# Performance work log

Measured on AMD Instinct MI355X. Metric: run time of the kernel, lower is better.

The kernel has to match this reference:

```python
import jax, jax.numpy as jnp
import numpy as np

R, N, C, E, H, NC = 25, 256, 64, 128, 8, 27


def _layernorm(x, w, b, axes, eps):
    m = x.mean(axis=axes, keepdims=True)
    v = x.var(axis=axes, keepdims=True)
    return (x - m) / jnp.sqrt(v + eps) * w + b


def _mha(emb_ln, idx, WQ, WK):
    # emb_ln: (R*N, E); idx: (L,) district indices
    ew = emb_ln.reshape(R, N, E)[idx]                       # (L,N,E) gather of district blocks
    Q = jnp.einsum('lne,hfe->lhnf', ew, WQ)                 # torch Linear: x @ W.T
    K = jnp.einsum('lne,hfe->lhnf', ew, WK)
    QK = jnp.einsum('lhnf,lhmf->lhnm', Q, K) / jnp.sqrt(jnp.float32(E))
    return jax.nn.softmax(QK, axis=2)                       # torch softmax(dim=1) over (L,n,n)


def setup_inputs() -> dict:
    key = jax.random.key(0)
    ks = jax.random.split(key, 16)
    inp = {
        'business_structure_target': jax.random.normal(ks[0], (R, C, N, 4), jnp.float32),
        'business_structure_infected': jax.random.normal(ks[1], (R, C, N, 4), jnp.float32),
        'customer_structure_target': jax.random.normal(ks[2], (R, C, N, NC, 4), jnp.float32),
        'customer_structure_infected': jax.random.normal(ks[3], (R, C, N, NC, 4), jnp.float32),
        'index_target_idx': jax.random.randint(ks[4], (R, C), 0, R),
        'index_infected_idx': jax.random.randint(ks[5], (R, C), 0, R),
        'covid_outbreak_business': jax.random.randint(ks[6], (R, C), 0, N),
        'emb_table': jax.random.normal(ks[7], (R * N, E), jnp.float32),
        'ln_emb_w': jnp.ones((E,), jnp.float32),
        'ln_emb_b': jnp.zeros((E,), jnp.float32),
        'WQ_trg': jax.random.normal(ks[8], (H, E, E), jnp.float32) * 0.05,
        'WK_trg': jax.random.normal(ks[9], (H, E, E), jnp.float32) * 0.05,
        'WQ_inf': jax.random.normal(ks[10], (H, E, E), jnp.float32) * 0.05,
        'WK_inf': jax.random.normal(ks[11], (H, E, E), jnp.float32) * 0.05,
        'W_os': jax.random.normal(ks[12], (E, E), jnp.float32) * 0.05,
        'b_os': jnp.zeros((E,), jnp.float32),
        'bs_w': jnp.ones((C, N), jnp.float32), 'bs_b': jnp.zeros((C, N), jnp.float32),
        'cs_w': jnp.ones((C, N), jnp.float32), 'cs_b': jnp.zeros((C, N), jnp.float32),
        'os_w': jnp.ones((C, N), jnp.float32), 'os_b': jnp.zeros((C, N), jnp.float32),
    }
    return inp


def reference(business_structure_target, business_structure_infected,
              customer_structure_target, customer_structure_infected,
              index_target_idx, index_infected_idx, covid_outbreak_business,
              emb_table, ln_emb_w, ln_emb_b,
              WQ_trg, WK_trg, WQ_inf, WK_inf,
              W_os, b_os, bs_w, bs_b, cs_w, cs_b, os_w, os_b):
    # mean over feature dim, then slicing per original forward
    bst = business_structure_target.mean(-1)[:R, 0]        # (R,N)
    bsi = business_structure_infected.mean(-1)[0]          # (C,N)
    cst = customer_structure_target.mean(-1)[:R, 0]        # (R,N,NC)
    csi = customer_structure_infected.mean(-1)[0]          # (C,N,NC)

    emb_ln = _layernorm(emb_table, ln_emb_w, ln_emb_b, -1, 1e-16)
    idx_t = index_target_idx[:R, 0]                        # (R,)
    idx_i = index_infected_idx[0]                          # (C,)

    attn_t = _mha(emb_ln, idx_t, WQ_trg, WK_trg)           # (R,H,N,N)
    BR_t = jnp.einsum('ln,lhnm->lmh', bst, attn_t)         # (R,N,H)
    attn_i = _mha(emb_ln, idx_i, WQ_inf, WK_inf)           # (C,H,N,N)
    BR_i = jnp.einsum('cn,chnm->cmh', bsi, attn_i)         # (C,N,H)

    # cosine similarity over head dim, broadcast (R,1,N,H) x (1,C,N,H)
    a = BR_t[:, None]
    b = BR_i[None]
    dot = jnp.sum(a * b, -1)
    na = jnp.linalg.norm(a, axis=-1)
    nb = jnp.linalg.norm(b, axis=-1)
    BS = dot / jnp.maximum(na * nb, 1e-15)                 # (R,C,N)

    # Jensen-Shannon-style KLD over consumer dim (log_target=True semantics)
    log_p = jax.nn.log_softmax(cst, -1)[:, None]           # (R,1,N,NC)
    log_q = jax.nn.log_softmax(csi, -1)[None]              # (1,C,N,NC)
    log_m = jax.nn.log_softmax((log_p + log_q) / 2, -1)
    kl_p = (jnp.exp(log_m) * (log_m - log_p)).mean(-1)
    kl_q = (jnp.exp(log_m) * (log_m - log_q)).mean(-1)
    CS = -(kl_p + kl_q) / 2                                # (R,C,N)

    biz = covid_outbreak_business[0]                       # (C,)
    inf_emb = emb_table[idx_i * N + biz]                   # (C,E) raw (non-LN) embedding
    proj = inf_emb @ W_os.T + b_os
    OS = (proj @ emb_table.T).reshape(C, R, N).transpose(1, 0, 2)  # (R,C,N)

    BS = _layernorm(BS, bs_w, bs_b, (-2, -1), 1e-5)
    CS = _layernorm(CS, cs_w, cs_b, (-2, -1), 1e-5)
    OS = _layernorm(OS, os_w, os_b, (-2, -1), 1e-5)
    return BS, CS, OS
```

## Files before the change

### kernel.cpp

```cpp
#include <hip/hip_runtime.h>
#include <math.h>

#define R_ 25
#define N_ 256
#define C_ 64
#define E_ 128
#define H_ 8
#define NC_ 27
#define SQS 28

typedef _Float16 f16x8 __attribute__((ext_vector_type(8)));
typedef float f32x16 __attribute__((ext_vector_type(16)));

union HU { ushort s; _Float16 h; };
__device__ __forceinline__ ushort ftoh(float f) { HU u; u.h = (_Float16)f; return u.s; }
__device__ __forceinline__ float htof(ushort s) { HU u; u.s = s; return (float)u.h; }

__device__ __forceinline__ float waveReduceSum(float v) {
  #pragma unroll
  for (int off = 32; off > 0; off >>= 1) v += __shfl_xor(v, off);
  return v;
}

__global__ __launch_bounds__(256) void k_prep(
    const float* __restrict__ emb, const float* __restrict__ ln_w,
    const float* __restrict__ ln_b, ushort* __restrict__ emb16,
    const float* __restrict__ bus_t, const float* __restrict__ bus_i,
    float* __restrict__ bst, float* __restrict__ bsi,
    const float* __restrict__ cus_t, const float* __restrict__ cus_i,
    float* __restrict__ Ssq, float* __restrict__ Tsq,
    const int* __restrict__ idx_t, const int* __restrict__ idx_i,
    int* __restrict__ cnt, int* __restrict__ lst,
    const int* __restrict__ biz, const float* __restrict__ Wos,
    const float* __restrict__ bos, float* __restrict__ projb) {
  __shared__ float er2[2][E_];
  int bid = blockIdx.x, t = threadIdx.x;
  if (bid < 1600) {
    int row = bid * 4 + (t >> 6);
    int lane = t & 63;
    const float2* x = (const float2*)(emb + (size_t)row * E_);
    float2 v = x[lane];
    float s = waveReduceSum(v.x + v.y);
    float m = s * (1.0f / 128.0f);
    float d0 = v.x - m, d1 = v.y - m;
    float ss = waveReduceSum(d0 * d0 + d1 * d1);
    float inv = 1.0f / sqrtf(ss * (1.0f / 128.0f) + 1e-16f);
    float2 wv = ((const float2*)ln_w)[lane];
    float2 bv = ((const float2*)ln_b)[lane];
    uint u = (uint)ftoh(d0 * inv * wv.x + bv.x) | ((uint)ftoh(d1 * inv * wv.y + bv.y) << 16);
    ((uint*)emb16)[(size_t)row * 64 + lane] = u;
  } else if (bid < 1689) {
    int i = (bid - 1600) * 256 + t;
    if (i < R_ * N_) {
      size_t row = (size_t)(i >> 8) * (C_ * N_) + (i & 255);
      float4 v = *(const float4*)&bus_t[row * 4];
      bst[i] = (v.x + v.y + v.z + v.w) * 0.25f;
    }
    int j = i - R_ * N_;
    if (j >= 0 && j < C_ * N_) {
      float4 v = *(const float4*)&bus_i[(size_t)j * 4];
      bsi[j] = (v.x + v.y + v.z + v.w) * 0.25f;
    }
  } else if (bid < 1778) {
    int i = (bid - 1689) * 256 + t;
    const float* src; float* dst; size_t base; int oi;
    if (i < R_ * N_) {
      src = cus_t; dst = Ssq; oi = i;
      base = ((size_t)(i >> 8) * (C_ * N_) + (i & 255)) * (NC_ * 4);
    } else {
      int j = i - R_ * N_;
      if (j >= C_ * N_) return;
      src = cus_i; dst = Tsq; oi = j;
      base = ((size_t)(j >> 8) * N_ + (j & 255)) * (NC_ * 4);
    }
    float v[NC_];
    float mx = -1e30f;
    #pragma unroll
    for (int j = 0; j < NC_; ++j) {
      float4 q = *(const float4*)&src[base + j * 4];
      v[j] = (q.x + q.y + q.z + q.w) * 0.25f;
      mx = fmaxf(mx, v[j]);
    }
    float se = 0.0f;
    #pragma unroll
    for (int j = 0; j < NC_; ++j) se += expf(v[j] - mx);
    float lse = mx + logf(se);
    #pragma unroll
    for (int j = 0; j < NC_; ++j) dst[(size_t)oi * SQS + j] = expf(0.5f * (v[j] - lse));
    dst[(size_t)oi * SQS + NC_] = 0.0f;
  } else if (bid == 1778) {
    if (t < 2 * R_) cnt[t] = 0;
    __syncthreads();
    if (t < R_) {
      int rr = idx_t[t * C_];
      int pos = atomicAdd(&cnt[rr], 1);
      lst[rr * 64 + pos] = t;
    }
    if (t < C_) {
      int rr = idx_i[t];
      int pos = atomicAdd(&cnt[R_ + rr], 1);
      lst[(R_ + rr) * 64 + pos] = t;
    }
  } else {
    int pb = bid - 1779;
    int ci = t >> 7, f = t & 127;
    int c = pb * 2 + ci;
    int row = idx_i[c] * N_ + biz[c];
    er2[ci][f] = emb[(size_t)row * E_ + f];
    __syncthreads();
    float acc = bos[f];
    const float* wr = &Wos[(size_t)f * E_];
    const float* er = er2[ci];
    for (int e = 0; e < E_; e += 4) {
      float4 w4 = *(const float4*)&wr[e];
      acc += er[e] * w4.x + er[e + 1] * w4.y + er[e + 2] * w4.z + er[e + 3] * w4.w;
    }
    projb[c * E_ + f] = acc;
  }
}

__global__ __launch_bounds__(512) void k_gt_mfma(
    const float* __restrict__ WQt_, const float* __restrict__ WKt_,
    const float* __restrict__ WQi_, const float* __restrict__ WKi_,
    ushort* __restrict__ Gt) {
  int h = blockIdx.x, set = blockIdx.y;
  const float* WQ = (set ? WQi_ : WQt_) + ((size_t)h << 14);
  const float* WK = (set ? WKi_ : WKt_) + ((size_t)h << 14);
  __shared__ uint QT[128 * 64];
  __shared__ uint KT[128 * 64];
  int t = threadIdx.x;
  for (int j = t; j < 8192; j += 512) {
    int e = j & 127, f2 = j >> 7;
    int wi = (f2 << 8) + e;
    float q0 = WQ[wi], q1 = WQ[wi + 128];
    float k0 = WK[wi], k1 = WK[wi + 128];
    int idx = (e << 6) + (f2 ^ ((e & 15) << 2));
    QT[idx] = (uint)ftoh(q0) | ((uint)ftoh(q1) << 16);
    KT[idx] = (uint)ftoh(k0) | ((uint)ftoh(k1) << 16);
  }
  __syncthreads();
  int w = t >> 6, l = t & 63, lo = l & 31, hi = l >> 5;
  int m0 = (w & 3) << 5, n0 = (w >> 2) << 6;
  f32x16 acc[2];
  #pragma unroll
  for (int i = 0; i < 2; ++i)
    #pragma unroll
    for (int j = 0; j < 16; ++j) acc[i][j] = 0.0f;
  int mrow = m0 + lo;
  #pragma unroll
  for (int ks = 0; ks < 8; ++ks) {
    int f2b = (ks << 3) + (hi << 2);
    f16x8 a = *(const f16x8*)&KT[(mrow << 6) + (f2b ^ ((mrow & 15) << 2))];
    #pragma unroll
    for (int tl = 0; tl < 2; ++tl) {
      int ncol = n0 + (tl << 5) + lo;
      f16x8 b = *(const f16x8*)&QT[(ncol << 6) + (f2b ^ ((ncol & 15) << 2))];
      acc[tl] = __builtin_amdgcn_mfma_f32_32x32x16_f16(a, b, acc[tl], 0, 0, 0);
    }
  }
  const float scale = 0.08838834764831845f;
  ushort* Go = Gt + (((size_t)(set * H_ + h)) << 14);
  #pragma unroll
  for (int tl = 0; tl < 2; ++tl)
    #pragma unroll
    for (int rg = 0; rg < 16; ++rg) {
      int row = m0 + (rg & 3) + ((rg >> 2) << 3) + (hi << 2);
      int col = n0 + (tl << 5) + lo;
      Go[(row << 7) + col] = ftoh(acc[tl][rg] * scale);
    }
}

__global__ __launch_bounds__(512) void k_attn_fused(
    const ushort* __restrict__ emb16, const ushort* __restrict__ GtAll,
    const int* __restrict__ cnt, const int* __restrict__ lst,
    const float* __restrict__ bst, const float* __restrict__ bsi,
    float* __restrict__ BRt, float* __restrict__ BRi) {
  int r = blockIdx.x, h = blockIdx.y, set = blockIdx.z;
  int g = set * R_ + r;
  int L = cnt[g];
  if (L == 0) return;
  __shared__ ushort ELN[256 * 128];
  __shared__ ushort TA[128 * 128];
  __shared__ ushort TB[128 * 128];
  __shared__ float redA[8 * 128];
  __shared__ float redB[8 * 128];
  __shared__ float gM[128], gD[128];
  int t = threadIdx.x;
  const uint4* Ep = (const uint4*)(emb16 + ((size_t)r << 15));
  for (int c = t; c < 4096; c += 512) {
    int n = c >> 4, s = c & 15;
    uint4 v = Ep[c];
    *(uint4*)&ELN[(n << 7) + ((s << 3) ^ ((n & 15) << 3))] = v;
  }
  const uint4* Gp = (const uint4*)(GtAll + ((size_t)(set * H_ + h) << 14));
  for (int c = t; c < 2048; c += 512) {
    int e2 = c >> 4, s = c & 15;
    uint4 v = Gp[c];
    *(uint4*)&TA[(e2 << 7) + ((s << 3) ^ ((e2 & 15) << 3))] = v;
  }
  __syncthreads();
  int w = t >> 6, l = t & 63, lo = l & 31, hi = l >> 5;
  f32x16 tacc[4];
  #pragma unroll
  for (int i = 0; i < 4; ++i)
    #pragma unroll
    for (int j = 0; j < 16; ++j) tacc[i][j] = 0.0f;
  int n = (w << 5) + lo;
  #pragma unroll
  for (int ks = 0; ks < 8; ++ks) {
    f16x8 a = *(const f16x8*)&ELN[(n << 7) + (((ks << 4) + (hi << 3)) ^ ((n & 15) << 3))];
    #pragma unroll
    for (int tl = 0; tl < 4; ++tl) {
      int f = (tl << 5) + lo;
      f16x8 b = *(const f16x8*)&TA[(f << 7) + (((ks << 4) + (hi << 3)) ^ ((f & 15) << 3))];
      tacc[tl] = __builtin_amdgcn_mfma_f32_32x32x16_f16(a, b, tacc[tl], 0, 0, 0);
    }
  }
  __syncthreads();
  {
    ushort* Tl = (w < 4) ? TA : TB;
    #pragma unroll
    for (int tl = 0; tl < 4; ++tl)
      #pragma unroll
      for (int rg = 0; rg < 16; ++rg) {
        int row = ((w & 3) << 5) + (rg & 3) + ((rg >> 2) << 3) + (hi << 2);
        int col = (tl << 5) + lo;
        Tl[(row << 7) + (col ^ ((row & 15) << 3))] = ftoh(tacc[tl][rg]);
      }
  }
  __syncthreads();
  const float* wv = set ? bsi : bst;
  float* BR = set ? BRi : BRt;
  const ushort* Tl = (w < 4) ? TA : TB;
  int rrow = n & 127;
  int baseRow = (w << 5) + (hi << 2);
  for (int mh = 0; mh < 2; ++mh) {
    f32x16 acc[4];
    #pragma unroll
    for (int i = 0; i < 4; ++i)
      #pragma unroll
      for (int j = 0; j < 16; ++j) acc[i][j] = 0.0f;
    #pragma unroll
    for (int ks = 0; ks < 8; ++ks) {
      f16x8 a = *(const f16x8*)&Tl[(rrow << 7) + (((ks << 4) + (hi << 3)) ^ ((rrow & 15) << 3))];
      #pragma unroll
      for (int tl = 0; tl < 4; ++tl) {
        int m = (mh << 7) + (tl << 5) + lo;
        f16x8 b = *(const f16x8*)&ELN[(m << 7) + (((ks << 4) + (hi << 3)) ^ ((m & 15) << 3))];
        acc[tl] = __builtin_amdgcn_mfma_f32_32x32x16_f16(a, b, acc[tl], 0, 0, 0);
      }
    }
    #pragma unroll
    for (int tl = 0; tl < 4; ++tl) {
      float mx = acc[tl][0];
      #pragma unroll
      for (int rg = 1; rg < 16; ++rg) mx = fmaxf(mx, acc[tl][rg]);
      mx = fmaxf(mx, __shfl_xor(mx, 32));
      if (hi == 0) redA[(w << 7) + (tl << 5) + lo] = mx;
    }
    __syncthreads();
    if (t < 128) {
      float gm = redA[t];
      #pragma unroll
      for (int ww = 1; ww < 8; ++ww) gm = fmaxf(gm, redA[(ww << 7) + t]);
      gM[t] = gm;
    }
    __syncthreads();
    #pragma unroll
    for (int tl = 0; tl < 4; ++tl) {
      float gmv = gM[(tl << 5) + lo];
      float s = 0.0f;
      #pragma unroll
      for (int rg = 0; rg < 16; ++rg) {
        acc[tl][rg] = __expf(acc[tl][rg] - gmv);
        s += acc[tl][rg];
      }
      s += __shfl_xor(s, 32);
      if (hi == 0) redB[(w << 7) + (tl << 5) + lo] = s;
    }
    __syncthreads();
    if (t < 128) {
      float d = 0.0f;
      #pragma unroll
      for (int ww = 0; ww < 8; ++ww) d += redB[(ww << 7) + t];
      gD[t] = d;
    }
    __syncthreads();
    for (int li = 0; li < L; ++li) {
      int ll = lst[g * 64 + li];
      float wreg[16];
      #pragma unroll
      for (int rg = 0; rg < 16; ++rg)
        wreg[rg] = wv[ll * N_ + baseRow + (rg & 3) + ((rg >> 2) << 3)];
      #pragma unroll
      for (int tl = 0; tl < 4; ++tl) {
        float part = 0.0f;
        #pragma unroll
        for (int rg = 0; rg < 16; ++rg) part += wreg[rg] * acc[tl][rg];
        part += __shfl_xor(part, 32);
        if (hi == 0) redA[(w << 7) + (tl << 5) + lo] = part;
      }
      __syncthreads();
      if (t < 128) {
        float s = 0.0f;
        #pragma unroll
        for (int ww = 0; ww < 8; ++ww) s += redA[(ww << 7) + t];
        BR[((size_t)ll * N_ + (mh << 7) + t) * H_ + h] = s / gD[t];
      }
      __syncthreads();
    }
  }
}

__global__ __launch_bounds__(256) void k_bscs_os(
    const float* __restrict__ BRt, const float* __restrict__ BRi,
    const float* __restrict__ Ssq, const float* __restrict__ Tsq,
    const float* __restrict__ emb, const float* __restrict__ projb,
    float* __restrict__ outBS, float* __restrict__ outCS,
    float* __restrict__ outOS) {
  __shared__ float pr[8][E_];
  int bid = blockIdx.x, t = threadIdx.x;
  if (bid < 1600) {
    int i = bid * 256 + t;
    int n = i & 255, c = (i >> 8) & 63, l = i >> 14;
    const float4* a = (const float4*)&BRt[((size_t)l * N_ + n) * H_];
    const float4* b = (const float4*)&BRi[((size_t)c * N_ + n) * H_];
    float4 a0 = a[0], a1 = a[1], b0 = b[0], b1 = b[1];
    float dot = a0.x * b0.x + a0.y * b0.y + a0.z * b0.z + a0.w * b0.w
              + a1.x * b1.x + a1.y * b1.y + a1.z * b1.z + a1.w * b1.w;
    float na = a0.x * a0.x + a0.y * a0.y + a0.z * a0.z + a0.w * a0.w
             + a1.x * a1.x + a1.y * a1.y + a1.z * a1.z + a1.w * a1.w;
    float nb = b0.x * b0.x + b0.y * b0.y + b0.z * b0.z + b0.w * b0.w
             + b1.x * b1.x + b1.y * b1.y + b1.z * b1.z + b1.w * b1.w;
    outBS[i] = dot / fmaxf(sqrtf(na) * sqrtf(nb), 1e-15f);

    const float4* sp = (const float4*)&Ssq[((size_t)l * N_ + n) * SQS];
    const float4* tp = (const float4*)&Tsq[((size_t)c * N_ + n) * SQS];
    float d2 = 0.0f;
    #pragma unroll
    for (int j = 0; j < 7; ++j) {
      float4 sv = sp[j], tv = tp[j];
      d2 += sv.x * tv.x + sv.y * tv.y + sv.z * tv.z + sv.w * tv.w;
    }
    outCS[i] = logf(d2) * (1.0f / 27.0f);
  } else {
    int o = bid - 1600;
    int l = o >> 3, cg = o & 7;
    for (int i = t; i < 1024; i += 256)
      pr[i >> 7][i & 127] = projb[(cg * 8 + (i >> 7)) * E_ + (i & 127)];
    __syncthreads();
    const float* er = &emb[((size_t)(l * N_) + t) << 7];
    float acc[8] = {0, 0, 0, 0, 0, 0, 0, 0};
    for (int e = 0; e < 128; e += 4) {
      float4 v = *(const float4*)&er[e];
      #pragma unroll
      for (int c = 0; c < 8; ++c)
        acc[c] += v.x * pr[c][e] + v.y * pr[c][e + 1] + v.z * pr[c][e + 2] + v.w * pr[c][e + 3];
    }
    #pragma unroll
    for (int c = 0; c < 8; ++c)
      outOS[((size_t)l * C_ + cg * 8 + c) * N_ + t] = acc[c];
  }
}

__global__ __launch_bounds__(1024) void k_ln_final(float* __restrict__ out,
    const float* __restrict__ w0, const float* __restrict__ b0,
    const float* __restrict__ w1, const float* __restrict__ b1,
    const float* __restrict__ w2, const float* __restrict__ b2) {
  int r = blockIdx.x, o = blockIdx.y;
  const float* w = (o == 0) ? w0 : ((o == 1) ? w1 : w2);
  const float* b = (o == 0) ? b0 : ((o == 1) ? b1 : b2);
  float* x = out + (size_t)o * 409600 + (size_t)r * 16384;
  int t = threadIdx.x;
  __shared__ float redm[16];
  float s = 0.0f;
  for (int i = t; i < 16384; i += 1024) s += x[i];
  s = waveReduceSum(s);
  if ((t & 63) == 0) redm[t >> 6] = s;
  __syncthreads();
  float m = 0.0f;
  #pragma unroll
  for (int k = 0; k < 16; ++k) m += redm[k];
  m *= (1.0f / 16384.0f);
  __syncthreads();
  float ss = 0.0f;
  for (int i = t; i < 16384; i += 1024) { float d = x[i] - m; ss += d * d; }
  ss = waveReduceSum(ss);
  if ((t & 63) == 0) redm[t >> 6] = ss;
  __syncthreads();
  float v = 0.0f;
  #pragma unroll
  for (int k = 0; k < 16; ++k) v += redm[k];
  v *= (1.0f / 16384.0f);
  float inv = 1.0f / sqrtf(v + 1e-5f);
  for (int i = t; i < 16384; i += 1024) x[i] = (x[i] - m) * inv * w[i] + b[i];
}

extern "C" void kernel_launch(void* const* d_in, const int* in_sizes, int n_in,
                              void* d_out, int out_size, void* d_ws, size_t ws_size,
                              hipStream_t stream) {
  const float* bus_t  = (const float*)d_in[0];
  const float* bus_i  = (const float*)d_in[1];
  const float* cus_t  = (const float*)d_in[2];
  const float* cus_i  = (const float*)d_in[3];
  const int*   idx_t  = (const int*)d_in[4];
  const int*   idx_i  = (const int*)d_in[5];
  const int*   cov    = (const int*)d_in[6];
  const float* emb    = (const float*)d_in[7];
  const float* ln_w   = (const float*)d_in[8];
  const float* ln_b   = (const float*)d_in[9];
  const float* WQ_trg = (const float*)d_in[10];
  const float* WK_trg = (const float*)d_in[11];
  const float* WQ_inf = (const float*)d_in[12];
  const float* WK_inf = (const float*)d_in[13];
  const float* W_os   = (const float*)d_in[14];
  const float* b_os   = (const float*)d_in[15];
  const float* bs_w   = (const float*)d_in[16];
  const float* bs_b   = (const float*)d_in[17];
  const float* cs_w   = (const float*)d_in[18];
  const float* cs_b   = (const float*)d_in[19];
  const float* os_w   = (const float*)d_in[20];
  const float* os_b   = (const float*)d_in[21];

  float* ws = (float*)d_ws;
  ushort* emb16 = (ushort*)ws;
  float* p = ws + 409600;
  ushort* Gt = (ushort*)p;   p += 131072;
  float* bst = p;            p += 6400;
  float* bsi = p;            p += 16384;
  float* Ssq = p;            p += R_ * N_ * SQS;
  float* Tsq = p;            p += C_ * N_ * SQS;
  float* BRt = p;            p += 51200;
  float* BRi = p;            p += 131072;
  float* projb = p;          p += 8192;
  int* cnt = (int*)p;        p += 64;
  int* lst = (int*)p;        p += 3200;

  float* outBS = (float*)d_out;
  float* outCS = outBS + 409600;
  float* outOS = outCS + 409600;

  k_prep<<<1811, 256, 0, stream>>>(emb, ln_w, ln_b, emb16,
                                   bus_t, bus_i, bst, bsi,
                                   cus_t, cus_i, Ssq, Tsq,
                                   idx_t, idx_i, cnt, lst,
                                   cov, W_os, b_os, projb);
  k_gt_mfma<<<dim3(H_, 2), 512, 0, stream>>>(WQ_trg, WK_trg, WQ_inf, WK_inf, Gt);
  k_attn_fused<<<dim3(R_, H_, 2), 512, 0, stream>>>(emb16, Gt, cnt, lst,
                                                    bst, bsi, BRt, BRi);
  k_bscs_os<<<1800, 256, 0, stream>>>(BRt, BRi, Ssq, Tsq, emb, projb,
                                      outBS, outCS, outOS);
  k_ln_final<<<dim3(R_, 3), 1024, 0, stream>>>(outBS, bs_w, bs_b, cs_w, cs_b, os_w, os_b);
}
```

Measured before the change: 84.19 us.

## Fuse Gt GEMM into prep, split softmax rows, compute LN stats in producer

The weight-product MFMA kernel is folded into the prep kernel as extra blocks, which saves one launch. The per-row customer softmax is now spread over four lanes with shuffle reductions, giving more parallelism on that memory-bound stage. The final layernorm no longer makes two reduction passes. The producer kernel emits per-block partial sums and sums of squares, and a wider apply kernel uses them. This adds the risk of precision loss from computing variance as E[x^2]-m^2 and increases LDS use in the prep kernel.

Result: no change. 84.56 us (+0.4%).

```diff
diff --git a/kernel.cpp b/kernel.cpp
--- a/kernel.cpp
+++ b/kernel.cpp
@@ -32,8 +32,11 @@
     const int* __restrict__ idx_t, const int* __restrict__ idx_i,
     int* __restrict__ cnt, int* __restrict__ lst,
     const int* __restrict__ biz, const float* __restrict__ Wos,
-    const float* __restrict__ bos, float* __restrict__ projb) {
-  __shared__ float er2[2][E_];
+    const float* __restrict__ bos, float* __restrict__ projb,
+    const float* __restrict__ WQt_, const float* __restrict__ WKt_,
+    const float* __restrict__ WQi_, const float* __restrict__ WKi_,
+    ushort* __restrict__ Gt) {
+  __shared__ uint sbuf[16384];
   int bid = blockIdx.x, t = threadIdx.x;
   if (bid < 1600) {
     int row = bid * 4 + (t >> 6);
@@ -61,34 +64,44 @@
       float4 v = *(const float4*)&bus_i[(size_t)j * 4];
       bsi[j] = (v.x + v.y + v.z + v.w) * 0.25f;
     }
-  } else if (bid < 1778) {
-    int i = (bid - 1689) * 256 + t;
+  } else if (bid < 2045) {
+    int gidx = (bid - 1689) * 256 + t;
+    int rowi = gidx >> 2, sub = gidx & 3;
     const float* src; float* dst; size_t base; int oi;
-    if (i < R_ * N_) {
-      src = cus_t; dst = Ssq; oi = i;
-      base = ((size_t)(i >> 8) * (C_ * N_) + (i & 255)) * (NC_ * 4);
+    if (rowi < R_ * N_) {
+      src = cus_t; dst = Ssq; oi = rowi;
+      base = ((size_t)(rowi >> 8) * (C_ * N_) + (rowi & 255)) * (NC_ * 4);
     } else {
-      int j = i - R_ * N_;
+      int j = rowi - R_ * N_;
       if (j >= C_ * N_) return;
       src = cus_i; dst = Tsq; oi = j;
       base = ((size_t)(j >> 8) * N_ + (j & 255)) * (NC_ * 4);
     }
-    float v[NC_];
+    int j0 = sub * 7;
+    int nj = (sub == 3) ? 6 : 7;
+    float v[7];
     float mx = -1e30f;
     #pragma unroll
-    for (int j = 0; j < NC_; ++j) {
-      float4 q = *(const float4*)&src[base + j * 4];
-      v[j] = (q.x + q.y + q.z + q.w) * 0.25f;
-      mx = fmaxf(mx, v[j]);
-    }
+    for (int k = 0; k < 7; ++k) {
+      if (k < nj) {
+        float4 q = *(const float4*)&src[base + (j0 + k) * 4];
+        v[k] = (q.x + q.y + q.z + q.w) * 0.25f;
+        mx = fmaxf(mx, v[k]);
+      }
+    }
+    mx = fmaxf(mx, __shfl_xor(mx, 1));
+    mx = fmaxf(mx, __shfl_xor(mx, 2));
     float se = 0.0f;
     #pragma unroll
-    for (int j = 0; j < NC_; ++j) se += expf(v[j] - mx);
+    for (int k = 0; k < 7; ++k) if (k < nj) se += expf(v[k] - mx);
+    se += __shfl_xor(se, 1);
+    se += __shfl_xor(se, 2);
     float lse = mx + logf(se);
     #pragma unroll
-    for (int j = 0; j < NC_; ++j) dst[(size_t)oi * SQS + j] = expf(0.5f * (v[j] - lse));
-    dst[(size_t)oi * SQS + NC_] = 0.0f;
-  } else if (bid == 1778) {
+    for (int k = 0; k < 7; ++k)
+      if (k < nj) dst[(size_t)oi * SQS + j0 + k] = expf(0.5f * (v[k] - lse));
+    if (sub == 3) dst[(size_t)oi * SQS + NC_] = 0.0f;
+  } else if (bid == 2045) {
     if (t < 2 * R_) cnt[t] = 0;
     __syncthreads();
     if (t < R_) {
@@ -101,73 +114,69 @@
       int pos = atomicAdd(&cnt[R_ + rr], 1);
       lst[(R_ + rr) * 64 + pos] = t;
     }
-  } else {
-    int pb = bid - 1779;
+  } else if (bid < 2078) {
+    float* er2 = (float*)sbuf;
+    int pb = bid - 2046;
     int ci = t >> 7, f = t & 127;
     int c = pb * 2 + ci;
     int row = idx_i[c] * N_ + biz[c];
-    er2[ci][f] = emb[(size_t)row * E_ + f];
+    er2[ci * E_ + f] = emb[(size_t)row * E_ + f];
     __syncthreads();
     float acc = bos[f];
     const float* wr = &Wos[(size_t)f * E_];
-    const float* er = er2[ci];
+    const float* er = &er2[ci * E_];
     for (int e = 0; e < E_; e += 4) {
       float4 w4 = *(const float4*)&wr[e];
       acc += er[e] * w4.x + er[e + 1] * w4.y + er[e + 2] * w4.z + er[e + 3] * w4.w;
     }
     projb[c * E_ + f] = acc;
-  }
-}
-
-__global__ __launch_bounds__(512) void k_gt_mfma(
-    const float* __restrict__ WQt_, const float* __restrict__ WKt_,
-    const float* __restrict__ WQi_, const float* __restrict__ WKi_,
-    ushort* __restrict__ Gt) {
-  int h = blockIdx.x, set = blockIdx.y;
-  const float* WQ = (set ? WQi_ : WQt_) + ((size_t)h << 14);
-  const float* WK = (set ? WKi_ : WKt_) + ((size_t)h << 14);
-  __shared__ uint QT[128 * 64];
-  __shared__ uint KT[128 * 64];
-  int t = threadIdx.x;
-  for (int j = t; j < 8192; j += 512) {
-    int e = j & 127, f2 = j >> 7;
-    int wi = (f2 << 8) + e;
-    float q0 = WQ[wi], q1 = WQ[wi + 128];
-    float k0 = WK[wi], k1 = WK[wi + 128];
-    int idx = (e << 6) + (f2 ^ ((e & 15) << 2));
-    QT[idx] = (uint)ftoh(q0) | ((uint)ftoh(q1) << 16);
-    KT[idx] = (uint)ftoh(k0) | ((uint)ftoh(k1) << 16);
-  }
-  __syncthreads();
-  int w = t >> 6, l = t & 63, lo = l & 31, hi = l >> 5;
-  int m0 = (w & 3) << 5, n0 = (w >> 2) << 6;
-  f32x16 acc[2];
-  #pragma unroll
-  for (int i = 0; i < 2; ++i)
-    #pragma unroll
-    for (int j = 0; j < 16; ++j) acc[i][j] = 0.0f;
-  int mrow = m0 + lo;
-  #pragma unroll
-  for (int ks = 0; ks < 8; ++ks) {
-    int f2b = (ks << 3) + (hi << 2);
-    f16x8 a = *(const f16x8*)&KT[(mrow << 6) + (f2b ^ ((mrow & 15) << 2))];
-    #pragma unroll
-    for (int tl = 0; tl < 2; ++tl) {
-      int ncol = n0 + (tl << 5) + lo;
-      f16x8 b = *(const f16x8*)&QT[(ncol << 6) + (f2b ^ ((ncol & 15) << 2))];
-      acc[tl] = __builtin_amdgcn_mfma_f32_32x32x16_f16(a, b, acc[tl], 0, 0, 0);
-    }
-  }
-  const float scale = 0.08838834764831845f;
-  ushort* Go = Gt + (((size_t)(set * H_ + h)) << 14);
-  #pragma unroll
-  for (int tl = 0; tl < 2; ++tl)
-    #pragma unroll
-    for (int rg = 0; rg < 16; ++rg) {
-      int row = m0 + (rg & 3) + ((rg >> 2) << 3) + (hi << 2);
-      int col = n0 + (tl << 5) + lo;
-      Go[(row << 7) + col] = ftoh(acc[tl][rg] * scale);
-    }
+  } else {
+    int gb = bid - 2078;
+    int h = gb & 7, set = gb >> 3;
+    const float* WQ = (set ? WQi_ : WQt_) + ((size_t)h << 14);
+    const float* WK = (set ? WKi_ : WKt_) + ((size_t)h << 14);
+    uint* QT = sbuf;
+    uint* KT = sbuf + 8192;
+    for (int j = t; j < 8192; j += 256) {
+      int e = j & 127, f2 = j >> 7;
+      int wi = (f2 << 8) + e;
+      float q0 = WQ[wi], q1 = WQ[wi + 128];
+      float k0 = WK[wi], k1 = WK[wi + 128];
+      int idx = (e << 6) + (f2 ^ ((e & 15) << 2));
+      QT[idx] = (uint)ftoh(q0) | ((uint)ftoh(q1) << 16);
+      KT[idx] = (uint)ftoh(k0) | ((uint)ftoh(k1) << 16);
+    }
+    __syncthreads();
+    int w = t >> 6, l = t & 63, lo = l & 31, hi = l >> 5;
+    int m0 = w << 5;
+    f32x16 acc[4];
+    #pragma unroll
+    for (int i = 0; i < 4; ++i)
+      #pragma unroll
+      for (int j = 0; j < 16; ++j) acc[i][j] = 0.0f;
+    int mrow = m0 + lo;
+    #pragma unroll
+    for (int ks = 0; ks < 8; ++ks) {
+      int f2b = (ks << 3) + (hi << 2);
+      f16x8 a = *(const f16x8*)&KT[(mrow << 6) + (f2b ^ ((mrow & 15) << 2))];
+      #pragma unroll
+      for (int tl = 0; tl < 4; ++tl) {
+        int ncol = (tl << 5) + lo;
+        f16x8 b = *(const f16x8*)&QT[(ncol << 6) + (f2b ^ ((ncol & 15) << 2))];
+        acc[tl] = __builtin_amdgcn_mfma_f32_32x32x16_f16(a, b, acc[tl], 0, 0, 0);
+      }
+    }
+    const float scale = 0.08838834764831845f;
+    ushort* Go = Gt + (((size_t)(set * H_ + h)) << 14);
+    #pragma unroll
+    for (int tl = 0; tl < 4; ++tl)
+      #pragma unroll
+      for (int rg = 0; rg < 16; ++rg) {
+        int row = m0 + (rg & 3) + ((rg >> 2) << 3) + (hi << 2);
+        int col = (tl << 5) + lo;
+        Go[(row << 7) + col] = ftoh(acc[tl][rg] * scale);
+      }
+  }
 }
 
 __global__ __launch_bounds__(512) void k_attn_fused(
@@ -317,8 +326,11 @@
     const float* __restrict__ Ssq, const float* __restrict__ Tsq,
     const float* __restrict__ emb, const float* __restrict__ projb,
     float* __restrict__ outBS, float* __restrict__ outCS,
-    float* __restrict__ outOS) {
+    float* __restrict__ outOS,
+    float2* __restrict__ pBS, float2* __restrict__ pCS,
+    float2* __restrict__ pOS) {
   __shared__ float pr[8][E_];
+  __shared__ float rb[4][4];
   int bid = blockIdx.x, t = threadIdx.x;
   if (bid < 1600) {
     int i = bid * 256 + t;
@@ -332,7 +344,8 @@
              + a1.x * a1.x + a1.y * a1.y + a1.z * a1.z + a1.w * a1.w;
     float nb = b0.x * b0.x + b0.y * b0.y + b0.z * b0.z + b0.w * b0.w
              + b1.x * b1.x + b1.y * b1.y + b1.z * b1.z + b1.w * b1.w;
-    outBS[i] = dot / fmaxf(sqrtf(na) * sqrtf(nb), 1e-15f);
+    float bsv = dot / fmaxf(sqrtf(na) * sqrtf(nb), 1e-15f);
+    outBS[i] = bsv;
 
     const float4* sp = (const float4*)&Ssq[((size_t)l * N_ + n) * SQS];
     const float4* tp = (const float4*)&Tsq[((size_t)c * N_ + n) * SQS];
@@ -342,7 +355,22 @@
       float4 sv = sp[j], tv = tp[j];
       d2 += sv.x * tv.x + sv.y * tv.y + sv.z * tv.z + sv.w * tv.w;
     }
-    outCS[i] = logf(d2) * (1.0f / 27.0f);
+    float csv = logf(d2) * (1.0f / 27.0f);
+    outCS[i] = csv;
+    float s0 = waveReduceSum(bsv), q0 = waveReduceSum(bsv * bsv);
+    float s1 = waveReduceSum(csv), q1 = waveReduceSum(csv * csv);
+    if ((t & 63) == 0) {
+      int wv = t >> 6;
+      rb[wv][0] = s0; rb[wv][1] = q0; rb[wv][2] = s1; rb[wv][3] = q1;
+    }
+    __syncthreads();
+    if (t == 0) {
+      float A = 0, B = 0, Cq = 0, D = 0;
+      #pragma unroll
+      for (int k = 0; k < 4; ++k) { A += rb[k][0]; B += rb[k][1]; Cq += rb[k][2]; D += rb[k][3]; }
+      pBS[bid] = make_float2(A, B);
+      pCS[bid] = make_float2(Cq, D);
+    }
   } else {
     int o = bid - 1600;
     int l = o >> 3, cg = o & 7;
@@ -357,43 +385,67 @@
       for (int c = 0; c < 8; ++c)
         acc[c] += v.x * pr[c][e] + v.y * pr[c][e + 1] + v.z * pr[c][e + 2] + v.w * pr[c][e + 3];
     }
-    #pragma unroll
-    for (int c = 0; c < 8; ++c)
+    float s = 0.0f, q = 0.0f;
+    #pragma unroll
+    for (int c = 0; c < 8; ++c) {
       outOS[((size_t)l * C_ + cg * 8 + c) * N_ + t] = acc[c];
+      s += acc[c];
+      q += acc[c] * acc[c];
+    }
+    s = waveReduceSum(s);
+    q = waveReduceSum(q);
+    if ((t & 63) == 0) { int wv = t >> 6; rb[wv][0] = s; rb[wv][1] = q; }
+    __syncthreads();
+    if (t == 0) {
+      float A = 0, B = 0;
+      #pragma unroll
+      for (int k = 0; k < 4; ++k) { A += rb[k][0]; B += rb[k][1]; }
+      pOS[o] = make_float2(A, B);
+    }
   }
 }
 
-__global__ __launch_bounds__(1024) void k_ln_final(float* __restrict__ out,
+__global__ __launch_bounds__(256) void k_ln_apply(
+    float* __restrict__ out,
+    const float2* __restrict__ pBS, const float2* __restrict__ pCS,
+    const float2* __restrict__ pOS,
     const float* __restrict__ w0, const float* __restrict__ b0,
     const float* __restrict__ w1, const float* __restrict__ b1,
     const float* __restrict__ w2, const float* __restrict__ b2) {
-  int r = blockIdx.x, o = blockIdx.y;
-  const float* w = (o == 0) ? w0 : ((o == 1) ? w1 : w2);
-  const float* b = (o == 0) ? b0 : ((o == 1) ? b1 : b2);
+  int r = blockIdx.x, o = blockIdx.y, chunk = blockIdx.z;
+  int t = threadIdx.x;
+  __shared__ float sm[2];
+  if (t < 64) {
+    float s = 0.0f, q = 0.0f;
+    if (o == 2) {
+      if (t < 8) { float2 v = pOS[r * 8 + t]; s = v.x; q = v.y; }
+    } else {
+      const float2* pp = (o == 0) ? pBS : pCS;
+      float2 v = pp[r * 64 + t]; s = v.x; q = v.y;
+    }
+    #pragma unroll
+    for (int off = 32; off > 0; off >>= 1) {
+      s += __shfl_xor(s, off);
+      q += __shfl_xor(q, off);
+    }
+    if (t == 0) {
+      float m = s * (1.0f / 16384.0f);
+      float v = q * (1.0f / 16384.0f) - m * m;
+      sm[0] = m;
+      sm[1] = 1.0f / sqrtf(v + 1e-5f);
+    }
+  }
+  __syncthreads();
+  float m = sm[0], inv = sm[1];
+  const float* w = (o == 0) ? w0 : (o == 1) ? w1 : w2;
+  const float* b = (o == 0) ? b0 : (o == 1) ? b1 : b2;
   float* x = out + (size_t)o * 409600 + (size_t)r * 16384;
-  int t = threadIdx.x;
-  __shared__ float redm[16];
-  float s = 0.0f;
-  for (int i = t; i < 16384; i += 1024) s += x[i];
-  s = waveReduceSum(s);
-  if ((t & 63) == 0) redm[t >> 6] = s;
-  __syncthreads();
-  float m = 0.0f;
+  int base = chunk * 2048;
   #pragma unroll
-  for (int k = 0; k < 16; ++k) m += redm[k];
-  m *= (1.0f / 16384.0f);
-  __syncthreads();
-  float ss = 0.0f;
-  for (int i = t; i < 16384; i += 1024) { float d = x[i] - m; ss += d * d; }
-  ss = waveReduceSum(ss);
-  if ((t & 63) == 0) redm[t >> 6] = ss;
-  __syncthreads();
-  float v = 0.0f;
-  #pragma unroll
-  for (int k = 0; k < 16; ++k) v += redm[k];
-  v *= (1.0f / 16384.0f);
-  float inv = 1.0f / sqrtf(v + 1e-5f);
-  for (int i = t; i < 16384; i += 1024) x[i] = (x[i] - m) * inv * w[i] + b[i];
+  for (int k = 0; k < 8; ++k) {
+    int pos = base + k * 256 + t;
+    x[pos] = (x[pos] - m) * inv * w[pos] + b[pos];
+  }
 }
 
 extern "C" void kernel_launch(void* const* d_in, const int* in_sizes, int n_in,
@@ -435,20 +487,24 @@
   float* projb = p;          p += 8192;
   int* cnt = (int*)p;        p += 64;
   int* lst = (int*)p;        p += 3200;
+  float2* pBS = (float2*)p;  p += 3200;
+  float2* pCS = (float2*)p;  p += 3200;
+  float2* pOS = (float2*)p;  p += 400;
 
   float* outBS = (float*)d_out;
   float* outCS = outBS + 409600;
   float* outOS = outCS + 409600;
 
-  k_prep<<<1811, 256, 0, stream>>>(emb, ln_w, ln_b, emb16,
+  k_prep<<<2094, 256, 0, stream>>>(emb, ln_w, ln_b, emb16,
                                    bus_t, bus_i, bst, bsi,
                                    cus_t, cus_i, Ssq, Tsq,
                                    idx_t, idx_i, cnt, lst,
-                                   cov, W_os, b_os, projb);
-  k_gt_mfma<<<dim3(H_, 2), 512, 0, stream>>>(WQ_trg, WK_trg, WQ_inf, WK_inf, Gt);
+                                   cov, W_os, b_os, projb,
+                                   WQ_trg, WK_trg, WQ_inf, WK_inf, Gt);
   k_attn_fused<<<dim3(R_, H_, 2), 512, 0, stream>>>(emb16, Gt, cnt, lst,
                                                     bst, bsi, BRt, BRi);
   k_bscs_os<<<1800, 256, 0, stream>>>(BRt, BRi, Ssq, Tsq, emb, projb,
-                                      outBS, outCS, outOS);
-  k_ln_final<<<dim3(R_, 3), 1024, 0, stream>>>(outBS, bs_w, bs_b, cs_w, cs_b, os_w, os_b);
+                                      outBS, outCS, outOS, pBS, pCS, pOS);
+  k_ln_apply<<<dim3(R_, 3, 8), 256, 0, stream>>>(outBS, pBS, pCS, pOS,
+                                                 bs_w, bs_b, cs_w, cs_b, os_w, os_b);
 }
```
